# Optimization experiments

Measured on AMD Instinct MI355X. Metric: run time of the kernel, lower is better.

## Reference

```python
import jax, jax.numpy as jnp
import numpy as np

N = 4096      # num_nodes (single graph; batch is all-zeros in the original when absent)
CIN = 1024    # in_channels
H = 1024      # hidden_channels
COUT = 512    # out_channels
R = 10        # nodevec rank (hardcoded in the module)
BN_EPS = 1e-5


def setup_inputs() -> dict:
    key = jax.random.key(0)
    ks = jax.random.split(key, 8)
    w = lambda k, shp: jax.random.normal(k, shp, dtype=jnp.float32) * 0.02
    return {
        "x": jax.random.normal(ks[0], (N, CIN), dtype=jnp.float32),
        "w_map": w(ks[1], (CIN, H)),
        "b_map": jnp.zeros((H,), jnp.float32),
        "nv1": jax.random.normal(ks[2], (N, R), dtype=jnp.float32),
        "nv2": jax.random.normal(ks[3], (R, N), dtype=jnp.float32),
        "w1": w(ks[4], (H, H)),
        "b1": jnp.zeros((H,), jnp.float32),
        "w2": w(ks[5], (H, COUT)),
        "b2": jnp.zeros((COUT,), jnp.float32),
        "bn1_g": jnp.ones((H,), jnp.float32),
        "bn1_b": jnp.zeros((H,), jnp.float32),
        "bn1_m": jnp.zeros((H,), jnp.float32),
        "bn1_v": jnp.ones((H,), jnp.float32),
        "bn2_g": jnp.ones((COUT,), jnp.float32),
        "bn2_b": jnp.zeros((COUT,), jnp.float32),
        "bn2_m": jnp.zeros((COUT,), jnp.float32),
        "bn2_v": jnp.ones((COUT,), jnp.float32),
        "w_attn": w(ks[6], (COUT, 1)),
        "b_attn": jnp.zeros((1,), jnp.float32),
    }


def _batchnorm_eval(h, g, b, m, v):
    # BatchNorm1d in eval mode: running stats
    return (h - m) * jax.lax.rsqrt(v + BN_EPS) * g + b


def reference(x, w_map, b_map, nv1, nv2, w1, b1, w2, b2,
              bn1_g, bn1_b, bn1_m, bn1_v, bn2_g, bn2_b, bn2_m, bn2_v,
              w_attn, b_attn):
    # feature mapping
    xm = jax.nn.relu(x @ w_map + b_map)                       # [N, H]
    # adaptive adjacency: softmax(relu(nv1 @ nv2), dim=1) -> strictly positive,
    # so nonzero() yields the fully dense edge list; we keep it dense.
    adp = jax.nn.softmax(jax.nn.relu(nv1 @ nv2), axis=1)      # [N, N]
    # gcn_norm (PyG GCNConv default): add unit self-loops, normalize by
    # column-degree^-1/2 on both sides.
    A = adp + jnp.eye(N, dtype=adp.dtype)                      # [N, N]
    deg = jnp.sum(A, axis=0)                                   # column sums (target degree)
    dinv = jnp.where(deg > 0, jax.lax.rsqrt(deg), 0.0)
    An = (dinv[:, None] * A) * dinv[None, :]                   # D^-1/2 A D^-1/2
    # GCNConv: out_i = sum_j An[j, i] * (x W)_j + bias  =>  An^T @ (X W) + b
    h = jax.nn.relu(An.T @ (xm @ w1) + b1)                     # conv1 + relu
    h = _batchnorm_eval(h, bn1_g, bn1_b, bn1_m, bn1_v)         # bn1 (dropout off in eval)
    h = jax.nn.relu(An.T @ (h @ w2) + b2)                      # conv2 + relu
    h = _batchnorm_eval(h, bn2_g, bn2_b, bn2_m, bn2_v)         # bn2
    # global_mean_pool with batch == zeros -> single-graph mean
    pooled = jnp.mean(h, axis=0, keepdims=True)                # [1, COUT]
    attn = jax.nn.sigmoid(pooled @ w_attn + b_attn)            # [1, 1]
    return pooled * attn                                       # [1, COUT]
```

## Files before the change

### kernel.cpp

```cpp
#include <hip/hip_runtime.h>

#define NN 4096
#define R_RANK 10

typedef __bf16 bf16x8 __attribute__((ext_vector_type(8)));
typedef float floatx4 __attribute__((ext_vector_type(4)));

__device__ __forceinline__ unsigned short f2bf(float f) {
    union { float f; unsigned int u; } v; v.f = f;
    unsigned int r = v.u + 0x7FFFu + ((v.u >> 16) & 1u);
    return (unsigned short)(r >> 16);
}
__device__ __forceinline__ void gll16(const void* g, void* l) {
    __builtin_amdgcn_global_load_lds(
        (const __attribute__((address_space(1))) unsigned int*)g,
        (__attribute__((address_space(3))) unsigned int*)l, 16, 0, 0);
}
template<int N>
__device__ __forceinline__ void wait_vm() {
    if constexpr (N == 0)       asm volatile("s_waitcnt vmcnt(0)" ::: "memory");
    else if constexpr (N == 3)  asm volatile("s_waitcnt vmcnt(3)" ::: "memory");
    else if constexpr (N == 4)  asm volatile("s_waitcnt vmcnt(4)" ::: "memory");
    else if constexpr (N == 6)  asm volatile("s_waitcnt vmcnt(6)" ::: "memory");
    else if constexpr (N == 8)  asm volatile("s_waitcnt vmcnt(8)" ::: "memory");
    else if constexpr (N == 9)  asm volatile("s_waitcnt vmcnt(9)" ::: "memory");
    else if constexpr (N == 12) asm volatile("s_waitcnt vmcnt(12)" ::: "memory");
    else static_assert(N < 0, "add vmcnt literal");
}

__global__ __launch_bounds__(256) void row_stats_kernel(
    const float* __restrict__ nv1, const float* __restrict__ nv2,
    float* __restrict__ rowmax, float* __restrict__ rowsum,
    float* __restrict__ deg, float* __restrict__ pooled)
{
    const int i0 = blockIdx.x * 4;
    const int tid = threadIdx.x;
    if (blockIdx.x < 16) deg[blockIdx.x * 256 + tid] = 0.f;
    if (blockIdx.x >= 16 && blockIdx.x < 18) pooled[(blockIdx.x - 16) * 256 + tid] = 0.f;
    __shared__ float a[4][R_RANK];
    if (tid < 4 * R_RANK) a[tid / R_RANK][tid % R_RANK] = nv1[i0 * R_RANK + tid];
    __syncthreads();

    float s[4][16];
    float mx[4] = {0.f, 0.f, 0.f, 0.f};
    #pragma unroll
    for (int t = 0; t < 16; ++t) {
        const int j = t * 256 + tid;
        float v[R_RANK];
        #pragma unroll
        for (int r = 0; r < R_RANK; ++r) v[r] = nv2[r * NN + j];
        #pragma unroll
        for (int q = 0; q < 4; ++q) {
            float acc = 0.f;
            #pragma unroll
            for (int r = 0; r < R_RANK; ++r) acc = fmaf(a[q][r], v[r], acc);
            acc = fmaxf(acc, 0.f);
            s[q][t] = acc;
            mx[q] = fmaxf(mx[q], acc);
        }
    }
    __shared__ float red[4][4];
    #pragma unroll
    for (int q = 0; q < 4; ++q) {
        float m = mx[q];
        #pragma unroll
        for (int off = 32; off > 0; off >>= 1) m = fmaxf(m, __shfl_down(m, off, 64));
        if ((tid & 63) == 0) red[q][tid >> 6] = m;
    }
    __syncthreads();
    #pragma unroll
    for (int q = 0; q < 4; ++q)
        mx[q] = fmaxf(fmaxf(red[q][0], red[q][1]), fmaxf(red[q][2], red[q][3]));
    __syncthreads();
    float sm[4] = {0.f, 0.f, 0.f, 0.f};
    #pragma unroll
    for (int t = 0; t < 16; ++t)
        #pragma unroll
        for (int q = 0; q < 4; ++q) sm[q] += __expf(s[q][t] - mx[q]);
    #pragma unroll
    for (int q = 0; q < 4; ++q) {
        float m = sm[q];
        #pragma unroll
        for (int off = 32; off > 0; off >>= 1) m += __shfl_down(m, off, 64);
        if ((tid & 63) == 0) red[q][tid >> 6] = m;
    }
    __syncthreads();
    if (tid < 4) {
        rowmax[i0 + tid] = mx[tid];
        rowsum[i0 + tid] = red[tid][0] + red[tid][1] + red[tid][2] + red[tid][3];
    }
}

__global__ __launch_bounds__(256) void col_sum_kernel(
    const float* __restrict__ nv1, const float* __restrict__ nv2,
    const float* __restrict__ rowmax, const float* __restrict__ rowsum,
    float* __restrict__ deg)
{
    const int tid = threadIdx.x;
    const int j = blockIdx.x * 256 + tid;
    const int i0 = blockIdx.y * 64;
    __shared__ float a[64][R_RANK];
    __shared__ float rm[64], rs[64];
    if (tid < 64) {
        rm[tid] = rowmax[i0 + tid];
        rs[tid] = 1.0f / rowsum[i0 + tid];
    }
    for (int t = tid; t < 64 * R_RANK; t += 256)
        a[t / R_RANK][t % R_RANK] = nv1[i0 * R_RANK + t];
    __syncthreads();

    float v[R_RANK];
    #pragma unroll
    for (int r = 0; r < R_RANK; ++r) v[r] = nv2[r * NN + j];
    float acc = 0.f;
    #pragma unroll 4
    for (int t = 0; t < 64; ++t) {
        float s = 0.f;
        #pragma unroll
        for (int r = 0; r < R_RANK; ++r) s = fmaf(a[t][r], v[r], s);
        s = fmaxf(s, 0.f);
        acc += __expf(s - rm[t]) * rs[t];
    }
    atomicAdd(&deg[j], acc);
}

__global__ __launch_bounds__(256) void an_build_kernel(
    const float* __restrict__ nv1, const float* __restrict__ nv2,
    const float* __restrict__ rowmax, const float* __restrict__ rowsum,
    const float* __restrict__ deg, unsigned short* __restrict__ AnT)
{
    const int tid = threadIdx.x;
    const int j = blockIdx.x * 256 + tid;
    const int i0 = blockIdx.y * 8;
    __shared__ float v2s[8][R_RANK];
    __shared__ float dis[8];
    if (tid < 8 * R_RANK) {
        const int r = tid / 8, t = tid % 8;
        v2s[t][r] = nv2[r * NN + i0 + t];
    }
    if (tid < 8) dis[tid] = rsqrtf(1.0f + deg[i0 + tid]);

    float a[R_RANK];
    #pragma unroll
    for (int r = 0; r < R_RANK; ++r) a[r] = nv1[j * R_RANK + r];
    const float rm = rowmax[j];
    const float rs = 1.0f / rowsum[j];
    const float dj = rsqrtf(1.0f + deg[j]);
    __syncthreads();

    #pragma unroll
    for (int t = 0; t < 8; ++t) {
        const int i = i0 + t;
        float s = 0.f;
        #pragma unroll
        for (int r = 0; r < R_RANK; ++r) s = fmaf(a[r], v2s[t][r], s);
        s = fmaxf(s, 0.f);
        const float adp = __expf(s - rm) * rs;
        const float val = (adp + ((i == j) ? 1.f : 0.f)) * dis[t] * dj;
        AnT[(size_t)i * NN + j] = f2bf(val);
    }
}

__global__ __launch_bounds__(256) void prep_kernel(
    const float* __restrict__ x, const float* __restrict__ w_map,
    const float* __restrict__ w1, const float* __restrict__ w2,
    unsigned short* __restrict__ xb, unsigned short* __restrict__ wmT,
    unsigned short* __restrict__ w1T, unsigned short* __restrict__ w2T)
{
    const int z = blockIdx.z;
    const int tid = threadIdx.x;
    if (z == 3) {
        const int b = blockIdx.x + blockIdx.y * 32;
        const size_t base = (size_t)b * 4096 + (size_t)tid * 16;
        #pragma unroll
        for (int i = 0; i < 2; ++i) {
            const float4 a0 = *(const float4*)(x + base + i * 8);
            const float4 a1 = *(const float4*)(x + base + i * 8 + 4);
            ushort4 p, q;
            p.x = f2bf(a0.x); p.y = f2bf(a0.y); p.z = f2bf(a0.z); p.w = f2bf(a0.w);
            q.x = f2bf(a1.x); q.y = f2bf(a1.y); q.z = f2bf(a1.z); q.w = f2bf(a1.w);
            *(ushort4*)(xb + base + i * 8) = p;
            *(ushort4*)(xb + base + i * 8 + 4) = q;
        }
        return;
    }
    const float* W = (z == 0) ? w_map : (z == 1) ? w1 : w2;
    unsigned short* WT = (z == 0) ? wmT : (z == 1) ? w1T : w2T;
    const int CN = (z == 2) ? 512 : 1024;
    if (blockIdx.x * 32 >= CN) return;
    __shared__ float s[32][33];
    const int tx = tid & 31, ty = tid >> 5;
    const int r0 = blockIdx.y * 32, c0 = blockIdx.x * 32;
    #pragma unroll
    for (int i = 0; i < 4; ++i)
        s[ty + 8 * i][tx] = W[(size_t)(r0 + ty + 8 * i) * CN + c0 + tx];
    __syncthreads();
    #pragma unroll
    for (int i = 0; i < 4; ++i)
        WT[(size_t)(c0 + ty + 8 * i) * 1024 + r0 + tx] = f2bf(s[tx][ty + 8 * i]);
}

template<int OUTM, int EPI, int SK>
__global__ __launch_bounds__(512) void gemm_mfma(
    const unsigned short* __restrict__ A, const unsigned short* __restrict__ Bt,
    void* __restrict__ Out, const int M, const int N, const int K,
    const float* __restrict__ bias, const float* __restrict__ gamma,
    const float* __restrict__ beta, const float* __restrict__ mean,
    const float* __restrict__ var)
{
    __shared__ __align__(16) unsigned short As[4][8192];
    __shared__ __align__(16) unsigned short Bs[4][8192];
    const int tid = threadIdx.x;
    const int l = tid & 63, w = tid >> 6;
    const int wy = w >> 2, wx = w & 3;
    const int lr = l & 15, lq = l >> 4;

    const int gx = gridDim.x, gy = gridDim.y;
    int lin = blockIdx.x + gx * (blockIdx.y + gy * blockIdx.z);
    const int q = (gx * gy * gridDim.z) >> 3;
    lin = (lin & 7) * q + (lin >> 3);
    const int bx = lin % gx;
    const int by = (lin / gx) % gy;
    const int bz = lin / (gx * gy);

    const int row0 = by * 128, col0 = bx * 128;
    const int Kc = K / SK;
    const int kb = bz * Kc;
    const int nt = Kc >> 6;

    const unsigned short* Ag0 = A + (size_t)(row0 + w * 16 + lr) * K + kb + lq * 8;
    const unsigned short* Bg0 = Bt + (size_t)(col0 + w * 16 + lr) * K + kb + lq * 8;

    floatx4 acc[4][2];
    #pragma unroll
    for (int i = 0; i < 4; ++i)
        #pragma unroll
        for (int j = 0; j < 2; ++j) acc[i][j] = (floatx4){0.f, 0.f, 0.f, 0.f};

    #define STAGE(b, t)                                                         \
    {                                                                           \
        char* Aw = (char*)As[b] + w * 1024;                                     \
        char* Bw = (char*)Bs[b] + w * 1024;                                     \
        const int kk = (t) * 64;                                                \
        gll16(Ag0 + kk,      Aw);                                               \
        gll16(Ag0 + kk + 32, Aw + 8192);                                        \
        gll16(Bg0 + kk,      Bw);                                               \
        gll16(Bg0 + kk + 32, Bw + 8192);                                        \
    }

    STAGE(0, 0)
    STAGE(1, 1)
    STAGE(2, 2)
    for (int t = 0; t < nt; ++t) {
        if (t + 3 < nt) {
            STAGE((t + 3) & 3, t + 3)
            wait_vm<12>();
        } else if (t + 2 < nt) {
            wait_vm<8>();
        } else if (t + 1 < nt) {
            wait_vm<4>();
        } else {
            wait_vm<0>();
        }
        __builtin_amdgcn_sched_barrier(0);
        __builtin_amdgcn_s_barrier();
        __builtin_amdgcn_sched_barrier(0);

        const char* Afr = (const char*)As[t & 3] + wy * 4096 + l * 16;
        const char* Bfr = (const char*)Bs[t & 3] + wx * 2048 + l * 16;
        #pragma unroll
        for (int h = 0; h < 2; ++h) {
            bf16x8 af[4], bf[2];
            #pragma unroll
            for (int i = 0; i < 4; ++i) af[i] = *(const bf16x8*)(Afr + h * 8192 + i * 1024);
            #pragma unroll
            for (int j = 0; j < 2; ++j) bf[j] = *(const bf16x8*)(Bfr + h * 8192 + j * 1024);
            #pragma unroll
            for (int mf = 0; mf < 4; ++mf)
                #pragma unroll
                for (int nf = 0; nf < 2; ++nf)
                    acc[mf][nf] = __builtin_amdgcn_mfma_f32_16x16x32_bf16(
                        af[mf], bf[nf], acc[mf][nf], 0, 0, 0);
        }
        __builtin_amdgcn_sched_barrier(0);
        __builtin_amdgcn_s_barrier();
        __builtin_amdgcn_sched_barrier(0);
    }
    #undef STAGE

    const int gr0 = row0 + wy * 64 + lq * 4;
    const int gc0 = col0 + wx * 32 + lr;
    if constexpr (OUTM == 0) {
        float* Pz = (float*)Out + (size_t)bz * M * N;
        #pragma unroll
        for (int mf = 0; mf < 4; ++mf) {
            const int gr = gr0 + mf * 16;
            #pragma unroll
            for (int nf = 0; nf < 2; ++nf) {
                const int gc = gc0 + nf * 16;
                #pragma unroll
                for (int r = 0; r < 4; ++r)
                    Pz[(size_t)(gr + r) * N + gc] = acc[mf][nf][r];
            }
        }
    } else {
        unsigned short* O = (unsigned short*)Out;
        #pragma unroll
        for (int nf = 0; nf < 2; ++nf) {
            const int gc = gc0 + nf * 16;
            float bb = 0.f, sc = 1.f, sh = 0.f;
            if constexpr (EPI >= 1) bb = bias[gc];
            if constexpr (EPI == 2) {
                sc = gamma[gc] * rsqrtf(var[gc] + 1e-5f);
                sh = beta[gc] - mean[gc] * sc;
            }
            #pragma unroll
            for (int mf = 0; mf < 4; ++mf) {
                const int gr = gr0 + mf * 16;
                #pragma unroll
                for (int r = 0; r < 4; ++r) {
                    float xv = acc[mf][nf][r];
                    if constexpr (EPI >= 1) xv = fmaxf(xv + bb, 0.f);
                    if constexpr (EPI == 2) xv = fmaf(xv, sc, sh);
                    O[(size_t)(gr + r) * N + gc] = f2bf(xv);
                }
            }
        }
    }
}

template<int BM, int BN, int SK>
__global__ __launch_bounds__(512, 1) void gemm_big(
    const unsigned short* __restrict__ A, const unsigned short* __restrict__ Bt,
    float* __restrict__ P, const int M, const int N, const int K)
{
    constexpr int MR = BM / 32;
    constexpr int NRF = BN / 64;
    constexpr int LPT = (BM + BN) / 128;
    constexpr int ABYTES = BM * 64;
    __shared__ __align__(16) unsigned short L[4][(BM + BN) * 32];
    const int tid = threadIdx.x;
    const int l = tid & 63, w = tid >> 6;
    const int wy = w >> 2, wx = w & 3;
    const int lr = l & 15, lq = l >> 4;

    const int gx = gridDim.x, gy = gridDim.y;
    int lin = blockIdx.x + gx * (blockIdx.y + gy * blockIdx.z);
    const int q = (gx * gy * gridDim.z) >> 3;
    lin = (lin & 7) * q + (lin >> 3);
    const int bx = lin % gx;
    const int by = (lin / gx) % gy;
    const int bz = lin / (gx * gy);

    const int row0 = by * BM, col0 = bx * BN;
    const int Kc = K / SK, kb = bz * Kc;
    const int nt = Kc >> 5;

    const unsigned short* Ag = A + (size_t)(row0 + w * (BM / 8) + lr) * K + kb + lq * 8;
    const unsigned short* Bg = Bt + (size_t)(col0 + w * (BN / 8) + lr) * K + kb + lq * 8;

    floatx4 acc[MR][NRF];
    #pragma unroll
    for (int i = 0; i < MR; ++i)
        #pragma unroll
        for (int j = 0; j < NRF; ++j) acc[i][j] = (floatx4){0.f, 0.f, 0.f, 0.f};

    #define STAGEB(b, t)                                                        \
    {                                                                           \
        char* Ld = (char*)L[b];                                                 \
        const int kk = (t) * 32;                                                \
        _Pragma("unroll")                                                       \
        for (int s = 0; s < BM / 128; ++s)                                      \
            gll16(Ag + (size_t)(s * 16) * K + kk,                               \
                  Ld + (w * (BM / 128) + s) * 1024);                            \
        _Pragma("unroll")                                                       \
        for (int s = 0; s < BN / 128; ++s)                                      \
            gll16(Bg + (size_t)(s * 16) * K + kk,                               \
                  Ld + ABYTES + (w * (BN / 128) + s) * 1024);                   \
    }

    STAGEB(0, 0)
    STAGEB(1, 1)
    STAGEB(2, 2)
    for (int t = 0; t < nt; ++t) {
        if (t + 3 < nt) {
            STAGEB((t + 3) & 3, t + 3)
            wait_vm<3 * LPT>();
        } else if (t + 2 < nt) {
            wait_vm<2 * LPT>();
        } else if (t + 1 < nt) {
            wait_vm<LPT>();
        } else {
            wait_vm<0>();
        }
        __builtin_amdgcn_sched_barrier(0);
        __builtin_amdgcn_s_barrier();
        __builtin_amdgcn_sched_barrier(0);

        const char* Ab = (const char*)L[t & 3] + wy * (MR * 1024) + l * 16;
        const char* Bb = (const char*)L[t & 3] + ABYTES + wx * (NRF * 1024) + l * 16;
        bf16x8 af[MR], bf[NRF];
        #pragma unroll
        for (int i = 0; i < MR; ++i) af[i] = *(const bf16x8*)(Ab + i * 1024);
        #pragma unroll
        for (int j = 0; j < NRF; ++j) bf[j] = *(const bf16x8*)(Bb + j * 1024);
        __builtin_amdgcn_s_setprio(1);
        #pragma unroll
        for (int mf = 0; mf < MR; ++mf)
            #pragma unroll
            for (int nf = 0; nf < NRF; ++nf)
                acc[mf][nf] = __builtin_amdgcn_mfma_f32_16x16x32_bf16(
                    af[mf], bf[nf], acc[mf][nf], 0, 0, 0);
        __builtin_amdgcn_s_setprio(0);
        __builtin_amdgcn_sched_barrier(0);
        __builtin_amdgcn_s_barrier();
        __builtin_amdgcn_sched_barrier(0);
    }
    #undef STAGEB

    float* Pz = P + (size_t)bz * M * N;
    const int gr0 = row0 + wy * (BM / 2) + lq * 4;
    const int gc0 = col0 + wx * (BN / 4) + lr;
    #pragma unroll
    for (int mf = 0; mf < MR; ++mf) {
        const int gr = gr0 + mf * 16;
        #pragma unroll
        for (int nf = 0; nf < NRF; ++nf) {
            const int gc = gc0 + nf * 16;
            #pragma unroll
            for (int r = 0; r < 4; ++r)
                Pz[(size_t)(gr + r) * N + gc] = acc[mf][nf][r];
        }
    }
}

template<int EPI, int S, int NC>
__global__ __launch_bounds__(256) void reduce_k(
    const float* __restrict__ P, unsigned short* __restrict__ out, const int MN,
    const float* __restrict__ bias, const float* __restrict__ gamma,
    const float* __restrict__ beta, const float* __restrict__ mean,
    const float* __restrict__ var)
{
    const int idx = blockIdx.x * 256 + threadIdx.x;
    const int n4 = MN >> 2;
    const float4* Pv = (const float4*)P;
    float4 v = Pv[idx];
    #pragma unroll
    for (int z = 1; z < S; ++z) {
        const float4 t = Pv[idx + (size_t)z * n4];
        v.x += t.x; v.y += t.y; v.z += t.z; v.w += t.w;
    }
    float vals[4] = {v.x, v.y, v.z, v.w};
    if constexpr (EPI >= 1) {
        const int c0 = (idx << 2) & (NC - 1);
        const float4 b4 = *(const float4*)(bias + c0);
        const float bb[4] = {b4.x, b4.y, b4.z, b4.w};
        float sc[4], sh[4];
        if constexpr (EPI == 2) {
            const float4 g4 = *(const float4*)(gamma + c0);
            const float4 e4 = *(const float4*)(beta + c0);
            const float4 m4 = *(const float4*)(mean + c0);
            const float4 v4 = *(const float4*)(var + c0);
            const float gg[4] = {g4.x, g4.y, g4.z, g4.w};
            const float ee[4] = {e4.x, e4.y, e4.z, e4.w};
            const float mm[4] = {m4.x, m4.y, m4.z, m4.w};
            const float vv[4] = {v4.x, v4.y, v4.z, v4.w};
            #pragma unroll
            for (int j = 0; j < 4; ++j) {
                sc[j] = gg[j] * rsqrtf(vv[j] + 1e-5f);
                sh[j] = ee[j] - mm[j] * sc[j];
            }
        }
        #pragma unroll
        for (int j = 0; j < 4; ++j) {
            float xv = fmaxf(vals[j] + bb[j], 0.f);
            if constexpr (EPI == 2) xv = fmaf(xv, sc[j], sh[j]);
            vals[j] = xv;
        }
    }
    ushort4 p;
    p.x = f2bf(vals[0]); p.y = f2bf(vals[1]); p.z = f2bf(vals[2]); p.w = f2bf(vals[3]);
    *(ushort4*)(out + ((size_t)idx << 2)) = p;
}

template<int S>
__global__ __launch_bounds__(256) void reduce_pool_kernel(
    const float* __restrict__ P, float* __restrict__ pooled,
    const float* __restrict__ bias, const float* __restrict__ gamma,
    const float* __restrict__ beta, const float* __restrict__ mean,
    const float* __restrict__ var)
{
    const int idx = blockIdx.x * 256 + threadIdx.x;
    const int row = blockIdx.x >> 2;
    constexpr int n4 = 512 * 4096 / 4;
    const float4* Pv = (const float4*)P;
    float4 v = Pv[idx];
    #pragma unroll
    for (int z = 1; z < S; ++z) {
        const float4 t = Pv[idx + (size_t)z * n4];
        v.x += t.x; v.y += t.y; v.z += t.z; v.w += t.w;
    }
    const float b0 = bias[row];
    const float sc = gamma[row] * rsqrtf(var[row] + 1e-5f);
    const float sh = beta[row] - mean[row] * sc;
    float s = 0.f;
    const float vals[4] = {v.x, v.y, v.z, v.w};
    #pragma unroll
    for (int j = 0; j < 4; ++j)
        s += fmaf(fmaxf(vals[j] + b0, 0.f), sc, sh);
    #pragma unroll
    for (int off = 32; off > 0; off >>= 1) s += __shfl_down(s, off, 64);
    __shared__ float red[4];
    if ((threadIdx.x & 63) == 0) red[threadIdx.x >> 6] = s;
    __syncthreads();
    if (threadIdx.x == 0)
        atomicAdd(&pooled[row], red[0] + red[1] + red[2] + red[3]);
}

__global__ __launch_bounds__(512) void finalize_kernel(
    const float* __restrict__ pooled, const float* __restrict__ w_attn,
    const float* __restrict__ b_attn, float* __restrict__ out)
{
    const int c = threadIdx.x;
    __shared__ float red[512];
    const float p = pooled[c] * (1.0f / 4096.0f);
    red[c] = p * w_attn[c];
    __syncthreads();
    for (int s = 256; s > 0; s >>= 1) {
        if (c < s) red[c] += red[c + s];
        __syncthreads();
    }
    const float attn = 1.0f / (1.0f + __expf(-(red[0] + b_attn[0])));
    out[c] = p * attn;
}

extern "C" void kernel_launch(void* const* d_in, const int* in_sizes, int n_in,
                              void* d_out, int out_size, void* d_ws, size_t ws_size,
                              hipStream_t stream) {
    const float* x      = (const float*)d_in[0];
    const float* w_map  = (const float*)d_in[1];
    const float* b_map  = (const float*)d_in[2];
    const float* nv1    = (const float*)d_in[3];
    const float* nv2    = (const float*)d_in[4];
    const float* w1     = (const float*)d_in[5];
    const float* b1     = (const float*)d_in[6];
    const float* w2     = (const float*)d_in[7];
    const float* b2     = (const float*)d_in[8];
    const float* bn1_g  = (const float*)d_in[9];
    const float* bn1_b  = (const float*)d_in[10];
    const float* bn1_m  = (const float*)d_in[11];
    const float* bn1_v  = (const float*)d_in[12];
    const float* bn2_g  = (const float*)d_in[13];
    const float* bn2_b  = (const float*)d_in[14];
    const float* bn2_m  = (const float*)d_in[15];
    const float* bn2_v  = (const float*)d_in[16];
    const float* w_attn = (const float*)d_in[17];
    const float* b_attn = (const float*)d_in[18];
    float* out = (float*)d_out;

    const size_t MB = 1024 * 1024;
    const bool big = ws_size >= 118 * MB;
    char* ws = (char*)d_ws;
    unsigned short* AnT = (unsigned short*)(ws);
    float*          P   = (float*)(ws + 32 * MB);
    char* B0 = big ? (ws + 96 * MB) : (ws + 64 * MB);
    unsigned short* xb  = (unsigned short*)(B0);
    unsigned short* t1T = (unsigned short*)(B0);
    unsigned short* t2T = (unsigned short*)(B0);
    unsigned short* xm  = (unsigned short*)(B0 + 8 * MB);
    unsigned short* h1  = (unsigned short*)(B0 + 8 * MB);
    unsigned short* wmT = (unsigned short*)(B0 + 16 * MB);
    unsigned short* w1T = (unsigned short*)(B0 + 18 * MB);
    unsigned short* w2T = (unsigned short*)(B0 + 20 * MB);
    float* deg    = (float*)(B0 + 21 * MB);
    float* rowmax = deg + 4096;
    float* rowsum = rowmax + 4096;
    float* pooled = rowsum + 4096;

    prep_kernel<<<dim3(32, 32, 4), 256, 0, stream>>>(x, w_map, w1, w2, xb, wmT, w1T, w2T);
    row_stats_kernel<<<1024, 256, 0, stream>>>(nv1, nv2, rowmax, rowsum, deg, pooled);
    col_sum_kernel<<<dim3(16, 64), 256, 0, stream>>>(nv1, nv2, rowmax, rowsum, deg);
    an_build_kernel<<<dim3(16, 512), 256, 0, stream>>>(nv1, nv2, rowmax, rowsum, deg, AnT);

    gemm_mfma<1, 1, 1><<<dim3(8, 32, 1), 512, 0, stream>>>(xb, wmT, xm,
        4096, 1024, 1024, b_map, nullptr, nullptr, nullptr, nullptr);
    gemm_mfma<1, 0, 1><<<dim3(32, 8, 1), 512, 0, stream>>>(w1T, xm, t1T,
        1024, 4096, 1024, nullptr, nullptr, nullptr, nullptr, nullptr);
    if (big) {
        gemm_big<256, 256, 4><<<dim3(4, 16, 4), 512, 0, stream>>>(AnT, t1T, P, 4096, 1024, 4096);
        reduce_k<2, 4, 1024><<<4096, 256, 0, stream>>>(P, h1, 4194304,
            b1, bn1_g, bn1_b, bn1_m, bn1_v);
    } else {
        gemm_big<256, 128, 2><<<dim3(8, 16, 2), 512, 0, stream>>>(AnT, t1T, P, 4096, 1024, 4096);
        reduce_k<2, 2, 1024><<<4096, 256, 0, stream>>>(P, h1, 4194304,
            b1, bn1_g, bn1_b, bn1_m, bn1_v);
    }
    gemm_mfma<0, 0, 2><<<dim3(32, 4, 2), 512, 0, stream>>>(w2T, h1, P,
        512, 4096, 1024, nullptr, nullptr, nullptr, nullptr, nullptr);
    reduce_k<0, 2, 1><<<2048, 256, 0, stream>>>(P, t2T, 2097152,
        nullptr, nullptr, nullptr, nullptr, nullptr);
    gemm_big<128, 256, 4><<<dim3(16, 4, 4), 512, 0, stream>>>(t2T, AnT, P, 512, 4096, 4096);
    reduce_pool_kernel<4><<<2048, 256, 0, stream>>>(
        P, pooled, b2, bn2_g, bn2_b, bn2_m, bn2_v);

    finalize_kernel<<<1, 512, 0, stream>>>(pooled, w_attn, b_attn, out);
}
```

Baseline: 309.0 us.

## Interleave prefetch with split MFMA phases and retune buffering and conv2 tiling

The big GEMM now splits each k-step into two MFMA halves and issues the A and B prefetch loads for step t+3 separately, one inside each half, so global loads overlap compute more finely. The smaller GEMM drops from four LDS buffers to two, cutting shared memory and allowing more blocks per CU at the cost of less prefetch depth. When the big path is selected, the second adjacency GEMM uses 256x256 tiles with split-K 8. This trades a larger partial-sum reduction for fewer, larger tiles.

```diff
diff --git a/kernel.cpp b/kernel.cpp
--- a/kernel.cpp
+++ b/kernel.cpp
@@ -23,10 +23,9 @@
     else if constexpr (N == 4)  asm volatile("s_waitcnt vmcnt(4)" ::: "memory");
     else if constexpr (N == 6)  asm volatile("s_waitcnt vmcnt(6)" ::: "memory");
     else if constexpr (N == 8)  asm volatile("s_waitcnt vmcnt(8)" ::: "memory");
-    else if constexpr (N == 9)  asm volatile("s_waitcnt vmcnt(9)" ::: "memory");
-    else if constexpr (N == 12) asm volatile("s_waitcnt vmcnt(12)" ::: "memory");
     else static_assert(N < 0, "add vmcnt literal");
 }
+#define SB __builtin_amdgcn_sched_barrier(0)
 
 __global__ __launch_bounds__(256) void row_stats_kernel(
     const float* __restrict__ nv1, const float* __restrict__ nv2,
@@ -208,8 +207,8 @@
     const float* __restrict__ beta, const float* __restrict__ mean,
     const float* __restrict__ var)
 {
-    __shared__ __align__(16) unsigned short As[4][8192];
-    __shared__ __align__(16) unsigned short Bs[4][8192];
+    __shared__ __align__(16) unsigned short As[2][8192];
+    __shared__ __align__(16) unsigned short Bs[2][8192];
     const int tid = threadIdx.x;
     const int l = tid & 63, w = tid >> 6;
     const int wy = w >> 2, wx = w & 3;
@@ -249,25 +248,17 @@
     }
 
     STAGE(0, 0)
-    STAGE(1, 1)
-    STAGE(2, 2)
     for (int t = 0; t < nt; ++t) {
-        if (t + 3 < nt) {
-            STAGE((t + 3) & 3, t + 3)
-            wait_vm<12>();
-        } else if (t + 2 < nt) {
-            wait_vm<8>();
-        } else if (t + 1 < nt) {
+        if (t + 1 < nt) {
+            STAGE((t + 1) & 1, t + 1)
             wait_vm<4>();
         } else {
             wait_vm<0>();
         }
-        __builtin_amdgcn_sched_barrier(0);
-        __builtin_amdgcn_s_barrier();
-        __builtin_amdgcn_sched_barrier(0);
-
-        const char* Afr = (const char*)As[t & 3] + wy * 4096 + l * 16;
-        const char* Bfr = (const char*)Bs[t & 3] + wx * 2048 + l * 16;
+        SB; __builtin_amdgcn_s_barrier(); SB;
+
+        const char* Afr = (const char*)As[t & 1] + wy * 4096 + l * 16;
+        const char* Bfr = (const char*)Bs[t & 1] + wx * 2048 + l * 16;
         #pragma unroll
         for (int h = 0; h < 2; ++h) {
             bf16x8 af[4], bf[2];
@@ -282,9 +273,7 @@
                     acc[mf][nf] = __builtin_amdgcn_mfma_f32_16x16x32_bf16(
                         af[mf], bf[nf], acc[mf][nf], 0, 0, 0);
         }
-        __builtin_amdgcn_sched_barrier(0);
-        __builtin_amdgcn_s_barrier();
-        __builtin_amdgcn_sched_barrier(0);
+        SB; __builtin_amdgcn_s_barrier(); SB;
     }
     #undef STAGE
 
@@ -336,7 +325,10 @@
 {
     constexpr int MR = BM / 32;
     constexpr int NRF = BN / 64;
-    constexpr int LPT = (BM + BN) / 128;
+    constexpr int MH = MR / 2;
+    constexpr int NA = BM / 128;
+    constexpr int NB = BN / 128;
+    constexpr int LPT = NA + NB;
     constexpr int ABYTES = BM * 64;
     __shared__ __align__(16) unsigned short L[4][(BM + BN) * 32];
     const int tid = threadIdx.x;
@@ -365,58 +357,67 @@
         #pragma unroll
         for (int j = 0; j < NRF; ++j) acc[i][j] = (floatx4){0.f, 0.f, 0.f, 0.f};
 
-    #define STAGEB(b, t)                                                        \
+    #define STAGE_A(b, t)                                                       \
     {                                                                           \
         char* Ld = (char*)L[b];                                                 \
         const int kk = (t) * 32;                                                \
         _Pragma("unroll")                                                       \
-        for (int s = 0; s < BM / 128; ++s)                                      \
-            gll16(Ag + (size_t)(s * 16) * K + kk,                               \
-                  Ld + (w * (BM / 128) + s) * 1024);                            \
+        for (int s = 0; s < NA; ++s)                                            \
+            gll16(Ag + (size_t)(s * 16) * K + kk, Ld + (w * NA + s) * 1024);    \
+    }
+    #define STAGE_B(b, t)                                                       \
+    {                                                                           \
+        char* Ld = (char*)L[b] + ABYTES;                                        \
+        const int kk = (t) * 32;                                                \
         _Pragma("unroll")                                                       \
-        for (int s = 0; s < BN / 128; ++s)                                      \
-            gll16(Bg + (size_t)(s * 16) * K + kk,                               \
-                  Ld + ABYTES + (w * (BN / 128) + s) * 1024);                   \
-    }
-
-    STAGEB(0, 0)
-    STAGEB(1, 1)
-    STAGEB(2, 2)
+        for (int s = 0; s < NB; ++s)                                            \
+            gll16(Bg + (size_t)(s * 16) * K + kk, Ld + (w * NB + s) * 1024);    \
+    }
+
+    STAGE_A(0, 0) STAGE_B(0, 0)
+    STAGE_A(1, 1) STAGE_B(1, 1)
+    STAGE_A(2, 2) STAGE_B(2, 2)
     for (int t = 0; t < nt; ++t) {
-        if (t + 3 < nt) {
-            STAGEB((t + 3) & 3, t + 3)
-            wait_vm<3 * LPT>();
-        } else if (t + 2 < nt) {
-            wait_vm<2 * LPT>();
-        } else if (t + 1 < nt) {
-            wait_vm<LPT>();
-        } else {
-            wait_vm<0>();
-        }
-        __builtin_amdgcn_sched_barrier(0);
-        __builtin_amdgcn_s_barrier();
-        __builtin_amdgcn_sched_barrier(0);
+        if (t + 2 < nt)      wait_vm<2 * LPT>();
+        else if (t + 1 < nt) wait_vm<LPT>();
+        else                 wait_vm<0>();
+        SB; __builtin_amdgcn_s_barrier(); SB;
 
         const char* Ab = (const char*)L[t & 3] + wy * (MR * 1024) + l * 16;
         const char* Bb = (const char*)L[t & 3] + ABYTES + wx * (NRF * 1024) + l * 16;
-        bf16x8 af[MR], bf[NRF];
-        #pragma unroll
-        for (int i = 0; i < MR; ++i) af[i] = *(const bf16x8*)(Ab + i * 1024);
+
+        bf16x8 bf[NRF], af0[MH];
         #pragma unroll
         for (int j = 0; j < NRF; ++j) bf[j] = *(const bf16x8*)(Bb + j * 1024);
+        #pragma unroll
+        for (int i = 0; i < MH; ++i) af0[i] = *(const bf16x8*)(Ab + i * 1024);
+        if (t + 3 < nt) STAGE_A((t + 3) & 3, t + 3)
         __builtin_amdgcn_s_setprio(1);
         #pragma unroll
-        for (int mf = 0; mf < MR; ++mf)
+        for (int mf = 0; mf < MH; ++mf)
             #pragma unroll
             for (int nf = 0; nf < NRF; ++nf)
                 acc[mf][nf] = __builtin_amdgcn_mfma_f32_16x16x32_bf16(
-                    af[mf], bf[nf], acc[mf][nf], 0, 0, 0);
+                    af0[mf], bf[nf], acc[mf][nf], 0, 0, 0);
         __builtin_amdgcn_s_setprio(0);
-        __builtin_amdgcn_sched_barrier(0);
-        __builtin_amdgcn_s_barrier();
-        __builtin_amdgcn_sched_barrier(0);
-    }
-    #undef STAGEB
+        SB; __builtin_amdgcn_s_barrier(); SB;
+
+        bf16x8 af1[MH];
+        #pragma unroll
+        for (int i = 0; i < MH; ++i) af1[i] = *(const bf16x8*)(Ab + (MH + i) * 1024);
+        if (t + 3 < nt) STAGE_B((t + 3) & 3, t + 3)
+        __builtin_amdgcn_s_setprio(1);
+        #pragma unroll
+        for (int mf = 0; mf < MH; ++mf)
+            #pragma unroll
+            for (int nf = 0; nf < NRF; ++nf)
+                acc[MH + mf][nf] = __builtin_amdgcn_mfma_f32_16x16x32_bf16(
+                    af1[mf], bf[nf], acc[MH + mf][nf], 0, 0, 0);
+        __builtin_amdgcn_s_setprio(0);
+        SB; __builtin_amdgcn_s_barrier(); SB;
+    }
+    #undef STAGE_A
+    #undef STAGE_B
 
     float* Pz = P + (size_t)bz * M * N;
     const int gr0 = row0 + wy * (BM / 2) + lq * 4;
@@ -599,9 +600,15 @@
         512, 4096, 1024, nullptr, nullptr, nullptr, nullptr, nullptr);
     reduce_k<0, 2, 1><<<2048, 256, 0, stream>>>(P, t2T, 2097152,
         nullptr, nullptr, nullptr, nullptr, nullptr);
-    gemm_big<128, 256, 4><<<dim3(16, 4, 4), 512, 0, stream>>>(t2T, AnT, P, 512, 4096, 4096);
-    reduce_pool_kernel<4><<<2048, 256, 0, stream>>>(
-        P, pooled, b2, bn2_g, bn2_b, bn2_m, bn2_v);
+    if (big) {
+        gemm_big<256, 256, 8><<<dim3(16, 2, 8), 512, 0, stream>>>(t2T, AnT, P, 512, 4096, 4096);
+        reduce_pool_kernel<8><<<2048, 256, 0, stream>>>(
+            P, pooled, b2, bn2_g, bn2_b, bn2_m, bn2_v);
+    } else {
+        gemm_big<128, 256, 4><<<dim3(16, 4, 4), 512, 0, stream>>>(t2T, AnT, P, 512, 4096, 4096);
+        reduce_pool_kernel<4><<<2048, 256, 0, stream>>>(
+            P, pooled, b2, bn2_g, bn2_b, bn2_m, bn2_v);
+    }
 
     finalize_kernel<<<1, 512, 0, stream>>>(pooled, w_attn, b_attn, out);
 }
```

New measurement: 312.0 us. Within noise of the previous version (+1.0%).

## Use one barrier per K-step with 2-ahead prefetch and retile second aggregation GEMM

Applied to the files above, without the earlier changes.

Both GEMM main loops now prefetch two stages ahead into the 4-slot LDS ring instead of three, which lets the trailing s_barrier after the MFMA block be removed, leaving one barrier per iteration. The second aggregation GEMM (An^T @ t2) is retiled to 256-row tiles with a larger split-K (8 or 4 depending on the `big` path), and the reduce/pool kernel is matched to the new split count. The aim is to cut synchronization overhead and improve tile reuse. The cost is a shallower prefetch, which may hide less load latency, and a larger partial-sum buffer to reduce.

```diff
diff --git a/kernel.cpp b/kernel.cpp
--- a/kernel.cpp
+++ b/kernel.cpp
@@ -23,10 +23,9 @@
     else if constexpr (N == 4)  asm volatile("s_waitcnt vmcnt(4)" ::: "memory");
     else if constexpr (N == 6)  asm volatile("s_waitcnt vmcnt(6)" ::: "memory");
     else if constexpr (N == 8)  asm volatile("s_waitcnt vmcnt(8)" ::: "memory");
-    else if constexpr (N == 9)  asm volatile("s_waitcnt vmcnt(9)" ::: "memory");
-    else if constexpr (N == 12) asm volatile("s_waitcnt vmcnt(12)" ::: "memory");
     else static_assert(N < 0, "add vmcnt literal");
 }
+#define SB __builtin_amdgcn_sched_barrier(0)
 
 __global__ __launch_bounds__(256) void row_stats_kernel(
     const float* __restrict__ nv1, const float* __restrict__ nv2,
@@ -250,21 +249,16 @@
 
     STAGE(0, 0)
     STAGE(1, 1)
-    STAGE(2, 2)
     for (int t = 0; t < nt; ++t) {
-        if (t + 3 < nt) {
-            STAGE((t + 3) & 3, t + 3)
-            wait_vm<12>();
-        } else if (t + 2 < nt) {
+        if (t + 2 < nt) {
+            STAGE((t + 2) & 3, t + 2)
             wait_vm<8>();
         } else if (t + 1 < nt) {
             wait_vm<4>();
         } else {
             wait_vm<0>();
         }
-        __builtin_amdgcn_sched_barrier(0);
-        __builtin_amdgcn_s_barrier();
-        __builtin_amdgcn_sched_barrier(0);
+        SB; __builtin_amdgcn_s_barrier(); SB;
 
         const char* Afr = (const char*)As[t & 3] + wy * 4096 + l * 16;
         const char* Bfr = (const char*)Bs[t & 3] + wx * 2048 + l * 16;
@@ -282,9 +276,6 @@
                     acc[mf][nf] = __builtin_amdgcn_mfma_f32_16x16x32_bf16(
                         af[mf], bf[nf], acc[mf][nf], 0, 0, 0);
         }
-        __builtin_amdgcn_sched_barrier(0);
-        __builtin_amdgcn_s_barrier();
-        __builtin_amdgcn_sched_barrier(0);
     }
     #undef STAGE
 
@@ -336,7 +327,9 @@
 {
     constexpr int MR = BM / 32;
     constexpr int NRF = BN / 64;
-    constexpr int LPT = (BM + BN) / 128;
+    constexpr int NA = BM / 128;
+    constexpr int NB = BN / 128;
+    constexpr int LPT = NA + NB;
     constexpr int ABYTES = BM * 64;
     __shared__ __align__(16) unsigned short L[4][(BM + BN) * 32];
     const int tid = threadIdx.x;
@@ -370,32 +363,26 @@
         char* Ld = (char*)L[b];                                                 \
         const int kk = (t) * 32;                                                \
         _Pragma("unroll")                                                       \
-        for (int s = 0; s < BM / 128; ++s)                                      \
-            gll16(Ag + (size_t)(s * 16) * K + kk,                               \
-                  Ld + (w * (BM / 128) + s) * 1024);                            \
+        for (int s = 0; s < NA; ++s)                                            \
+            gll16(Ag + (size_t)(s * 16) * K + kk, Ld + (w * NA + s) * 1024);    \
         _Pragma("unroll")                                                       \
-        for (int s = 0; s < BN / 128; ++s)                                      \
+        for (int s = 0; s < NB; ++s)                                            \
             gll16(Bg + (size_t)(s * 16) * K + kk,                               \
-                  Ld + ABYTES + (w * (BN / 128) + s) * 1024);                   \
+                  Ld + ABYTES + (w * NB + s) * 1024);                           \
     }
 
     STAGEB(0, 0)
     STAGEB(1, 1)
-    STAGEB(2, 2)
     for (int t = 0; t < nt; ++t) {
-        if (t + 3 < nt) {
-            STAGEB((t + 3) & 3, t + 3)
-            wait_vm<3 * LPT>();
-        } else if (t + 2 < nt) {
+        if (t + 2 < nt) {
+            STAGEB((t + 2) & 3, t + 2)
             wait_vm<2 * LPT>();
         } else if (t + 1 < nt) {
             wait_vm<LPT>();
         } else {
             wait_vm<0>();
         }
-        __builtin_amdgcn_sched_barrier(0);
-        __builtin_amdgcn_s_barrier();
-        __builtin_amdgcn_sched_barrier(0);
+        SB; __builtin_amdgcn_s_barrier(); SB;
 
         const char* Ab = (const char*)L[t & 3] + wy * (MR * 1024) + l * 16;
         const char* Bb = (const char*)L[t & 3] + ABYTES + wx * (NRF * 1024) + l * 16;
@@ -412,9 +399,6 @@
                 acc[mf][nf] = __builtin_amdgcn_mfma_f32_16x16x32_bf16(
                     af[mf], bf[nf], acc[mf][nf], 0, 0, 0);
         __builtin_amdgcn_s_setprio(0);
-        __builtin_amdgcn_sched_barrier(0);
-        __builtin_amdgcn_s_barrier();
-        __builtin_amdgcn_sched_barrier(0);
     }
     #undef STAGEB
 
@@ -599,9 +583,15 @@
         512, 4096, 1024, nullptr, nullptr, nullptr, nullptr, nullptr);
     reduce_k<0, 2, 1><<<2048, 256, 0, stream>>>(P, t2T, 2097152,
         nullptr, nullptr, nullptr, nullptr, nullptr);
-    gemm_big<128, 256, 4><<<dim3(16, 4, 4), 512, 0, stream>>>(t2T, AnT, P, 512, 4096, 4096);
-    reduce_pool_kernel<4><<<2048, 256, 0, stream>>>(
-        P, pooled, b2, bn2_g, bn2_b, bn2_m, bn2_v);
+    if (big) {
+        gemm_big<256, 256, 8><<<dim3(16, 2, 8), 512, 0, stream>>>(t2T, AnT, P, 512, 4096, 4096);
+        reduce_pool_kernel<8><<<2048, 256, 0, stream>>>(
+            P, pooled, b2, bn2_g, bn2_b, bn2_m, bn2_v);
+    } else {
+        gemm_big<256, 128, 4><<<dim3(32, 2, 4), 512, 0, stream>>>(t2T, AnT, P, 512, 4096, 4096);
+        reduce_pool_kernel<4><<<2048, 256, 0, stream>>>(
+            P, pooled, b2, bn2_g, bn2_b, bn2_m, bn2_v);
+    }
 
     finalize_kernel<<<1, 512, 0, stream>>>(pooled, w_attn, b_attn, out);
 }
```

Result: faster. 294.1 us (median of 2 runs) (-4.8%).
